# Optimization experiments

Measured on AMD Instinct MI355X. Metric: run time of the kernel, lower is better.

## Reference

```python
import jax, jax.numpy as jnp
import numpy as np

EPS = 1e-5
K_NN = 16

def _lin1d(x, W, b):
    # 1x1 Conv1d: x (B,C,N) -> (B,O,N)
    return jnp.einsum('oc,bcn->bon', W, x) + b[None, :, None]

def _lin2d(x, W, b):
    # 1x1 Conv2d: x (B,C,N,K) -> (B,O,N,K)
    return jnp.einsum('oc,bcnk->bonk', W, x) + b[None, :, None, None]

def _bn2d(x, gamma, beta):
    # train-mode BatchNorm2d over (B, N, K) per channel
    mean = jnp.mean(x, axis=(0, 2, 3), keepdims=True)
    var = jnp.var(x, axis=(0, 2, 3), keepdims=True)
    xh = (x - mean) * jax.lax.rsqrt(var + EPS)
    return gamma[None, :, None, None] * xh + beta[None, :, None, None]

def _knn_idx(pq, ps, k):
    # pq (B,3,N), ps (B,3,M) -> idx (B,N,K) of k nearest support points
    d2 = (jnp.sum(pq * pq, axis=1)[:, :, None]
          + jnp.sum(ps * ps, axis=1)[:, None, :]
          - 2.0 * jnp.einsum('bcn,bcm->bnm', pq, ps))
    _, idx = jax.lax.top_k(-d2, k)
    return idx

def _group(x, idx):
    # x (B,C,M), idx (B,N,K) -> (B,C,N,K)
    return jnp.take_along_axis(x[:, :, None, :], idx[:, None, :, :], axis=3)

def setup_inputs() -> dict:
    key = jax.random.key(0)
    ks = jax.random.split(key, 20)
    B, C, D, N, M, H = 4, 128, 64, 2048, 2048, 256
    s = lambda k, shape, scale: (jax.random.normal(k, shape, dtype=jnp.float32) * scale)
    return {
        'pq': s(ks[0], (B, 3, N), 1.0),
        'fq': s(ks[1], (B, C, N), 1.0),
        'ps': s(ks[2], (B, 3, M), 1.0),
        'fs': s(ks[3], (B, C, M), 1.0),
        'Wq': s(ks[4], (D, C), 0.05), 'bq': jnp.zeros((D,), jnp.float32),
        'Wk': s(ks[5], (D, C), 0.05), 'bk': jnp.zeros((D,), jnp.float32),
        'Wv': s(ks[6], (D, C), 0.05), 'bv': jnp.zeros((D,), jnp.float32),
        'Wp1': s(ks[7], (D, 3), 0.2), 'bp1': jnp.zeros((D,), jnp.float32),
        'gp': jnp.ones((D,), jnp.float32), 'btp': jnp.zeros((D,), jnp.float32),
        'Wp2': s(ks[8], (D, D), 0.05), 'bp2': jnp.zeros((D,), jnp.float32),
        'Wa1': s(ks[9], (H, D), 0.05), 'ba1': jnp.zeros((H,), jnp.float32),
        'ga': jnp.ones((H,), jnp.float32), 'bta': jnp.zeros((H,), jnp.float32),
        'Wa2': s(ks[10], (D, H), 0.05), 'ba2': jnp.zeros((D,), jnp.float32),
        'We': s(ks[11], (C, D), 0.05), 'be': jnp.zeros((C,), jnp.float32),
    }

def reference(pq, fq, ps, fs, Wq, bq, Wk, bk, Wv, bv,
              Wp1, bp1, gp, btp, Wp2, bp2,
              Wa1, ba1, ga, bta, Wa2, ba2, We, be):
    identity = fq
    q = _lin1d(fq, Wq, bq)          # (B,D,N)
    k = _lin1d(fs, Wk, bk)          # (B,D,M)
    v = _lin1d(fs, Wv, bv)          # (B,D,M)
    idx = _knn_idx(pq, ps, K_NN)    # (B,N,K)
    key_g = _group(k, idx)          # (B,D,N,K)
    qk_rel = q[:, :, :, None] - key_g
    pos_rel = pq[:, :, :, None] - _group(ps, idx)  # (B,3,N,K)
    # pos_mlp: conv-bn-relu-conv
    pe = _lin2d(pos_rel, Wp1, bp1)
    pe = jax.nn.relu(_bn2d(pe, gp, btp))
    pe = _lin2d(pe, Wp2, bp2)       # (B,D,N,K)
    # attn_mlp: conv-bn-relu-conv
    a = _lin2d(qk_rel + pe, Wa1, ba1)
    a = jax.nn.relu(_bn2d(a, ga, bta))
    a = _lin2d(a, Wa2, ba2)         # (B,D,N,K)
    attn = jax.nn.softmax(a, axis=-1)
    val = _group(v, idx) + pe       # (B,D,N,K)
    agg = jnp.einsum('bcnk,bcnk->bcn', attn, val)
    return _lin1d(agg, We, be) + identity
```

## Files before the change

kernel.cpp:

```cpp
#include <hip/hip_runtime.h>
#include <stdint.h>

#define NN 2048
#define MM 2048
#define NSAMP 131072

typedef float  fv4 __attribute__((ext_vector_type(4)));
typedef short  bfv8 __attribute__((ext_vector_type(8)));
typedef short  bfv4 __attribute__((ext_vector_type(4)));
typedef unsigned short u16;
typedef unsigned long long u64;

__device__ inline u16 f2bf(float x){
  unsigned u = __float_as_uint(x);
  return (u16)((u + 0x7FFFu + ((u>>16)&1u)) >> 16);
}
__device__ inline float bf2f(u16 u){ return __uint_as_float(((unsigned)u)<<16); }
__device__ inline bfv8 ld8f(const float* __restrict__ p){
  fv4 a = *(const fv4*)p;
  fv4 b = *(const fv4*)(p + 4);
  bfv8 r;
  r[0]=(short)f2bf(a.x); r[1]=(short)f2bf(a.y); r[2]=(short)f2bf(a.z); r[3]=(short)f2bf(a.w);
  r[4]=(short)f2bf(b.x); r[5]=(short)f2bf(b.y); r[6]=(short)f2bf(b.z); r[7]=(short)f2bf(b.w);
  return r;
}
#define MFMA16 __builtin_amdgcn_mfma_f32_16x16x32_bf16

__global__ __launch_bounds__(256) void k_qkv(
    const float* __restrict__ fq, const float* __restrict__ fs,
    const float* __restrict__ Wq, const float* __restrict__ Wk, const float* __restrict__ Wv,
    const float* __restrict__ bq, const float* __restrict__ bk, const float* __restrict__ bv,
    const float* __restrict__ ps,
    float* __restrict__ qT, float* __restrict__ kT, float* __restrict__ vT,
    fv4* __restrict__ psP) {
  __shared__ u16 tile[2][32 * 136];
  int bid = blockIdx.x;
  int b = bid >> 6, p0 = (bid & 63) * 32;
  int t = threadIdx.x;
  int w = t >> 6, l = t & 63, lq = l >> 4, ln = l & 15;
  {
    int gid = bid * 256 + t;
    if (gid < 8192) { int bb = gid >> 11, m = gid & 2047;
      float x = ps[(bb*3+0)*MM + m], y = ps[(bb*3+1)*MM + m], z = ps[(bb*3+2)*MM + m];
      fv4 p; p.x = x; p.y = y; p.z = z; p.w = x*x + y*y + z*z;
      psP[gid] = p; }
  }
  {
    int cq = t >> 3, n4 = (t & 7) * 4;
    #pragma unroll
    for (int it = 0; it < 4; ++it) {
      int c = it * 32 + cq;
      fv4 vq = *(const fv4*)&fq[(b*128 + c)*2048 + p0 + n4];
      fv4 vs = *(const fv4*)&fs[(b*128 + c)*2048 + p0 + n4];
      #pragma unroll
      for (int j = 0; j < 4; ++j) {
        tile[0][(n4 + j)*136 + c] = f2bf(vq[j]);
        tile[1][(n4 + j)*136 + c] = f2bf(vs[j]);
      }
    }
  }
  bfv8 A[3][4];
  #pragma unroll
  for (int mat = 0; mat < 3; ++mat) {
    const float* W = mat == 0 ? Wq : (mat == 1 ? Wk : Wv);
    #pragma unroll
    for (int kk = 0; kk < 4; ++kk)
      A[mat][kk] = ld8f(W + (w*16 + ln)*128 + kk*32 + lq*8);
  }
  __syncthreads();
  fv4 acc[3][2];
  #pragma unroll
  for (int mat = 0; mat < 3; ++mat) {
    const u16* tl = tile[mat == 0 ? 0 : 1];
    #pragma unroll
    for (int nt = 0; nt < 2; ++nt) {
      fv4 a = {0.f,0.f,0.f,0.f};
      #pragma unroll
      for (int kk = 0; kk < 4; ++kk) {
        bfv8 bb = *(const bfv8*)&tl[(nt*16 + ln)*136 + kk*32 + lq*8];
        a = MFMA16(A[mat][kk], bb, a, 0, 0, 0);
      }
      acc[mat][nt] = a;
    }
  }
  #pragma unroll
  for (int mat = 0; mat < 3; ++mat) {
    float* dst = mat == 0 ? qT : (mat == 1 ? kT : vT);
    const float* bia = mat == 0 ? bq : (mat == 1 ? bk : bv);
    fv4 bq4 = *(const fv4*)&bia[w*16 + lq*4];
    #pragma unroll
    for (int nt = 0; nt < 2; ++nt) {
      fv4 o = acc[mat][nt] + bq4;
      *(fv4*)&dst[(b*NN + p0 + nt*16 + ln)*64 + w*16 + lq*4] = o;
    }
  }
}

__global__ __launch_bounds__(256) void k_knn(
    const float* __restrict__ pq, const fv4* __restrict__ psP,
    int* __restrict__ idxb, float* __restrict__ posPart) {
  __shared__ u64 list[4][512];
  __shared__ u64 win[4][16];
  __shared__ int cnt[4];
  __shared__ float sacc[4][9];

  const int t = threadIdx.x, w = t >> 6, lane = t & 63;
  const int qi = blockIdx.x * 4 + w;
  const int b = qi >> 11, n = qi & 2047;
  const float* pqb = pq + b * 3 * NN;
  const fv4* psb = psP + b * 2048;
  const float qx = pqb[n], qy = pqb[NN + n], qz = pqb[2 * NN + n];
  const float qq = qx * qx + qy * qy + qz * qz;

  unsigned key[32];
  unsigned bkey = 0xFFFFFFFFu; unsigned bj = 0;
  #pragma unroll
  for (int j = 0; j < 32; ++j) {
    fv4 P = psb[lane + 64*j];
    float d2 = qq + P.w - 2.f * (qx * P.x + qy * P.y + qz * P.z);
    unsigned bu = __float_as_uint(d2);
    bu = (bu & 0x80000000u) ? ~bu : (bu | 0x80000000u);
    key[j] = bu;
    if (bu < bkey) { bkey = bu; bj = (unsigned)j; }
  }
  u64 e = (((u64)bkey) << 32) | (unsigned)(lane + 64*(int)bj);

  #pragma unroll
  for (int k = 2; k <= 64; k <<= 1) {
    #pragma unroll
    for (int j = k >> 1; j > 0; j >>= 1) {
      u64 x = __shfl_xor(e, j, 64);
      u64 lo = e < x ? e : x, hi = e < x ? x : e;
      bool up = ((lane & k) == 0);
      bool takeLo = (((lane & j) == 0) == up);
      e = takeLo ? lo : hi;
    }
  }
  const u64 thr = __shfl(e, 15, 64);
  const unsigned T32 = (unsigned)(thr >> 32);

  if (lane == 0) cnt[w] = 0;
  #pragma unroll
  for (int j = 0; j < 32; ++j) {
    if (key[j] <= T32) {
      int p = atomicAdd(&cnt[w], 1);
      if (p < 512) list[w][p] = (((u64)key[j]) << 32) | (unsigned)(lane + 64*j);
    }
  }
  const int C = *(volatile int*)&cnt[w];

  u64 myWin = 0;
  if (C <= 64) {
    u64 v = (lane < C) ? list[w][lane] : ~0ULL;
    #pragma unroll
    for (int k = 2; k <= 64; k <<= 1) {
      #pragma unroll
      for (int j = k >> 1; j > 0; j >>= 1) {
        u64 x = __shfl_xor(v, j, 64);
        u64 lo = v < x ? v : x, hi = v < x ? x : v;
        bool up = ((lane & k) == 0);
        bool takeLo = (((lane & j) == 0) == up);
        v = takeLo ? lo : hi;
      }
    }
    myWin = v;
  } else if (C <= 128) {
    u64 e0 = list[w][lane];
    u64 e1 = (64 + lane < C) ? list[w][64 + lane] : ~0ULL;
    #pragma unroll
    for (unsigned k = 2; k <= 128; k <<= 1) {
      #pragma unroll
      for (unsigned j = k >> 1; j > 0; j >>= 1) {
        if (j < 64) {
          u64 x0 = __shfl_xor(e0, (int)j, 64);
          u64 x1 = __shfl_xor(e1, (int)j, 64);
          bool lower = ((lane & j) == 0);
          bool up0 = (k == 128) ? true : ((lane & k) == 0);
          bool up1 = (k == 128) ? true : ((k == 64) ? false : ((lane & k) == 0));
          e0 = (lower == up0) ? (e0 < x0 ? e0 : x0) : (e0 < x0 ? x0 : e0);
          e1 = (lower == up1) ? (e1 < x1 ? e1 : x1) : (e1 < x1 ? x1 : e1);
        } else {
          u64 lo = e0 < e1 ? e0 : e1, hi = e0 < e1 ? e1 : e0;
          e0 = lo; e1 = hi;
        }
      }
    }
    myWin = e0;
  } else {
    int Cc = C > 512 ? 512 : C;
    for (int i = lane; i < 512; i += 64)
      if (i >= Cc) list[w][i] = ~0ULL;
    for (int r = 0; r < 16; ++r) {
      u64 mv = ~0ULL;
      #pragma unroll
      for (int s5 = 0; s5 < 8; ++s5) {
        u64 x = list[w][s5*64 + lane];
        mv = x < mv ? x : mv;
      }
      #pragma unroll
      for (int off = 1; off <= 32; off <<= 1) {
        u64 x = __shfl_xor(mv, off, 64);
        mv = x < mv ? x : mv;
      }
      #pragma unroll
      for (int s5 = 0; s5 < 8; ++s5)
        if (list[w][s5*64 + lane] == mv) list[w][s5*64 + lane] = ~0ULL;
      if (lane == 0) win[w][r] = mv;
    }
    if (lane < 16) myWin = win[w][lane];
  }

  if (lane < 16) {
    unsigned m = (unsigned)(myWin & 0xFFFFFFFFu);
    idxb[qi * 16 + lane] = (int)m;
    fv4 P = psb[m];
    float r0 = qx - P.x, r1 = qy - P.y, r2 = qz - P.z;
    float s[9];
    s[0] = r0; s[1] = r1; s[2] = r2;
    s[3] = r0*r0; s[4] = r0*r1; s[5] = r0*r2;
    s[6] = r1*r1; s[7] = r1*r2; s[8] = r2*r2;
    #pragma unroll
    for (int off = 1; off <= 8; off <<= 1)
      #pragma unroll
      for (int i = 0; i < 9; ++i) s[i] += __shfl_xor(s[i], off, 64);
    if (lane == 0)
      #pragma unroll
      for (int i = 0; i < 9; ++i) sacc[w][i] = s[i];
  }
  __syncthreads();
  if (t < 9) posPart[blockIdx.x * 12 + t]
      = sacc[0][t] + sacc[1][t] + sacc[2][t] + sacc[3][t];
}

__global__ __launch_bounds__(256) void k_posfinal(
    const float* __restrict__ Wp1, const float* __restrict__ bp1,
    const float* __restrict__ gp, const float* __restrict__ btp,
    const float* __restrict__ posPart, float* __restrict__ Wp1f, float* __restrict__ bp1f) {
  __shared__ float red[4][9];
  __shared__ float st[9];
  int t = threadIdx.x;
  int w = t >> 6, lane = t & 63;
  float s[9];
  #pragma unroll
  for (int i = 0; i < 9; ++i) s[i] = 0.f;
  #pragma unroll
  for (int it = 0; it < 8; ++it) {
    const float* p = posPart + (it * 256 + t) * 12;
    fv4 a = *(const fv4*)p;
    fv4 b4 = *(const fv4*)(p + 4);
    float c8 = p[8];
    s[0]+=a.x; s[1]+=a.y; s[2]+=a.z; s[3]+=a.w;
    s[4]+=b4.x; s[5]+=b4.y; s[6]+=b4.z; s[7]+=b4.w;
    s[8]+=c8;
  }
  #pragma unroll
  for (int off = 32; off > 0; off >>= 1)
    #pragma unroll
    for (int i = 0; i < 9; ++i) s[i] += __shfl_xor(s[i], off, 64);
  if (lane == 0)
    #pragma unroll
    for (int i = 0; i < 9; ++i) red[w][i] = s[i];
  __syncthreads();
  if (t < 9) st[t] = red[0][t] + red[1][t] + red[2][t] + red[3][t];
  __syncthreads();
  if (t < 64) {
    int d = t;
    const float invN = 1.f / (float)NSAMP;
    float m0 = st[0]*invN, m1 = st[1]*invN, m2 = st[2]*invN;
    float C00 = st[3]*invN - m0*m0, C01 = st[4]*invN - m0*m1, C02 = st[5]*invN - m0*m2;
    float C11 = st[6]*invN - m1*m1, C12 = st[7]*invN - m1*m2, C22 = st[8]*invN - m2*m2;
    float w0 = Wp1[d*3], w1 = Wp1[d*3+1], w2 = Wp1[d*3+2];
    float mean = w0*m0 + w1*m1 + w2*m2 + bp1[d];
    float var = w0*w0*C00 + w1*w1*C11 + w2*w2*C22 + 2.f*(w0*w1*C01 + w0*w2*C02 + w1*w2*C12);
    float scale = gp[d] * rsqrtf(var + 1e-5f);
    Wp1f[d*3]   = scale * w0;
    Wp1f[d*3+1] = scale * w1;
    Wp1f[d*3+2] = scale * w2;
    bp1f[d] = btp[d] + scale * (bp1[d] - mean);
  }
}

__global__ __launch_bounds__(256) void k_ystats(
    const float* __restrict__ pq, const float* __restrict__ ps,
    const float* __restrict__ qT, const float* __restrict__ kT,
    const int* __restrict__ idxb,
    const float* __restrict__ Wp1f, const float* __restrict__ bp1f,
    const float* __restrict__ Wp2, const float* __restrict__ bp2,
    float* __restrict__ Gpart, float* __restrict__ ySumPart) {
  __shared__ __align__(16) unsigned char smem[21760];
  u16*   hp   = (u16*)smem;
  u16*   y2   = (u16*)(smem + 9216);
  float* r3   = (float*)(smem + 18432);
  float* qc   = (float*)(smem + 19200);
  int*   idxA = (int*)(smem + 20224);
  float* sWp1 = (float*)(smem + 20480);
  float* sbp1 = (float*)(smem + 21248);
  float* sbp2 = (float*)(smem + 21504);

  const int t = threadIdx.x;
  const int w = t >> 6, l = t & 63, lq = l >> 4, ln = l & 15;
  const int d0 = 16*w + lq*4;

  if (t < 192) sWp1[t] = Wp1f[t];
  if (t < 64){ sbp1[t] = bp1f[t]; sbp2[t] = bp2[t]; }

  bfv8 Ape[2];
  #pragma unroll
  for (int kk = 0; kk < 2; ++kk)
    Ape[kk] = ld8f(Wp2 + (16*w + ln)*64 + kk*32 + lq*8);

  fv4 gacc[4];
  #pragma unroll
  for (int nt = 0; nt < 4; ++nt) gacc[nt] = (fv4){0.f,0.f,0.f,0.f};
  float ys[4] = {0.f, 0.f, 0.f, 0.f};
  __syncthreads();

  for (int ch = 0; ch < 4; ++ch) {
    const int p0 = blockIdx.x * 16 + ch * 4;
    const int b  = p0 >> 11;
    const int bN = b * 2048;
    if (t < 64) idxA[t] = idxb[p0*16 + t];
    qc[t] = qT[(p0 + (t>>6))*64 + (t & 63)];
    __syncthreads();
    if (t < 192) { int c = t >> 6, s = t & 63; int n = (p0 + (s>>4)) & 2047;
      r3[c*64 + s] = pq[(b*3+c)*NN + n] - ps[(b*3+c)*MM + idxA[s]]; }
    __syncthreads();
    { int s = t >> 2, iq = t & 3;
      float r0 = r3[s], r1 = r3[64+s], r2 = r3[128+s];
      u16 tmp[16];
      #pragma unroll
      for (int e = 0; e < 16; ++e) { int i = iq*16 + e;
        float v = sbp1[i] + sWp1[i*3]*r0 + sWp1[i*3+1]*r1 + sWp1[i*3+2]*r2;
        tmp[e] = f2bf(fmaxf(v, 0.f)); }
      *(bfv8*)&hp[s*72 + iq*16]     = *(const bfv8*)&tmp[0];
      *(bfv8*)&hp[s*72 + iq*16 + 8] = *(const bfv8*)&tmp[8];
    }
    __syncthreads();
    {
      fv4 pe[4];
      #pragma unroll
      for (int nt = 0; nt < 4; ++nt) {
        fv4 acc = {0.f,0.f,0.f,0.f};
        #pragma unroll
        for (int kk = 0; kk < 2; ++kk) {
          bfv8 bb = *(const bfv8*)&hp[(nt*16 + ln)*72 + kk*32 + lq*8];
          acc = MFMA16(Ape[kk], bb, acc, 0, 0, 0);
        }
        pe[nt] = acc;
      }
      fv4 bp2q = *(const fv4*)&sbp2[d0];
      #pragma unroll
      for (int nt = 0; nt < 4; ++nt) {
        int s = nt*16 + ln;
        int mi = idxA[s];
        fv4 kg = *(const fv4*)(kT + (bN + mi)*64 + d0);
        fv4 qv = *(const fv4*)&qc[nt*64 + d0];
        fv4 yv = qv - kg + pe[nt] + bp2q;
        #pragma unroll
        for (int r = 0; r < 4; ++r) { y2[(d0 + r)*72 + s] = f2bf(yv[r]); ys[r] += yv[r]; }
      }
    }
    __syncthreads();
    #pragma unroll
    for (int kk = 0; kk < 2; ++kk) {
      bfv8 aa = *(const bfv8*)&y2[(16*w + ln)*72 + kk*32 + lq*8];
      #pragma unroll
      for (int nt = 0; nt < 4; ++nt) {
        bfv8 bb = *(const bfv8*)&y2[(nt*16 + ln)*72 + kk*32 + lq*8];
        gacc[nt] = MFMA16(aa, bb, gacc[nt], 0, 0, 0);
      }
    }
    __syncthreads();
  }
  #pragma unroll
  for (int nt = 0; nt < 4; ++nt)
    #pragma unroll
    for (int r = 0; r < 4; ++r)
      Gpart[blockIdx.x*4096 + (16*w + lq*4 + r)*64 + nt*16 + ln] = gacc[nt][r];
  #pragma unroll
  for (int off = 1; off <= 8; off <<= 1) {
    #pragma unroll
    for (int r = 0; r < 4; ++r) ys[r] += __shfl_xor(ys[r], off, 64);
  }
  if (ln == 0) {
    #pragma unroll
    for (int r = 0; r < 4; ++r) ySumPart[blockIdx.x*64 + d0 + r] = ys[r];
  }
}

__global__ __launch_bounds__(256) void k_gred(
    const float* __restrict__ Gpart, const float* __restrict__ ySumPart,
    float* __restrict__ G, float* __restrict__ ySum) {
  __shared__ float red[256];
  int bid = blockIdx.x, t = threadIdx.x;
  int tj = t & 63, st = t >> 6;
  if (bid < 64) {
    int j = bid * 64 + tj;
    float s = 0.f;
    for (int p = st * 128; p < st * 128 + 128; ++p)
      s += Gpart[p*4096 + j];
    red[st * 64 + tj] = s;
    __syncthreads();
    if (t < 64)
      G[bid * 64 + t] = red[t] + red[64 + t] + red[128 + t] + red[192 + t];
  } else {
    float s = 0.f;
    for (int p = st * 128; p < st * 128 + 128; ++p)
      s += ySumPart[p*64 + tj];
    red[st * 64 + tj] = s;
    __syncthreads();
    if (t < 64)
      ySum[t] = red[t] + red[64 + t] + red[128 + t] + red[192 + t];
  }
}

__global__ __launch_bounds__(256) void k_attnfinal(
    const float* __restrict__ Wa1, const float* __restrict__ ba1,
    const float* __restrict__ ga, const float* __restrict__ bta,
    const float* __restrict__ ySum, const float* __restrict__ G,
    u16* __restrict__ Wa1fbf, float* __restrict__ ba1f) {
  __shared__ float red[256];
  __shared__ float mu[64];
  __shared__ float sc[1];
  int h = blockIdx.x, t = threadIdx.x;
  const float invN = 1.f / (float)NSAMP;
  if (t < 64) mu[t] = ySum[t] * invN;
  __syncthreads();
  float acc = 0.f;
  #pragma unroll
  for (int e = 0; e < 16; ++e) {
    int pi = t*16 + e, i = pi >> 6, j = pi & 63;
    float cov = G[pi]*invN - mu[i]*mu[j];
    acc += Wa1[h*64 + i] * Wa1[h*64 + j] * cov;
  }
  red[t] = acc;
  __syncthreads();
  for (int s = 128; s > 0; s >>= 1) { if (t < s) red[t] += red[t + s]; __syncthreads(); }
  float var = red[0];
  __syncthreads();
  red[t] = (t < 64) ? Wa1[h*64 + t] * mu[t] : 0.f;
  __syncthreads();
  for (int s = 128; s > 0; s >>= 1) { if (t < s) red[t] += red[t + s]; __syncthreads(); }
  if (t == 0) {
    float mean  = red[0] + ba1[h];
    float scale = ga[h] * rsqrtf(var + 1e-5f);
    sc[0] = scale;
    ba1f[h] = bta[h] + scale * (ba1[h] - mean);
  }
  __syncthreads();
  if (t < 64) Wa1fbf[h*64 + t] = f2bf(sc[0] * Wa1[h*64 + t]);
}

__global__ __launch_bounds__(256) void k_main(
    const float* __restrict__ pq, const float* __restrict__ ps,
    const float* __restrict__ qT, const float* __restrict__ kT, const float* __restrict__ vT,
    const int* __restrict__ idxb,
    const float* __restrict__ Wp1f, const float* __restrict__ bp1f,
    const float* __restrict__ Wp2, const float* __restrict__ bp2,
    const u16* __restrict__ Wa1fbf, const float* __restrict__ ba1f,
    const float* __restrict__ Wa2, const float* __restrict__ ba2,
    const float* __restrict__ We, const float* __restrict__ be,
    const float* __restrict__ fq,
    u16* __restrict__ aggbf, float* __restrict__ out) {
  __shared__ __align__(16) unsigned char smem[65024];
  u16*   hp   = (u16*)smem;
  u16*   ha   = (u16*)smem;
  u16*   ylds = (u16*)(smem + 33792);
  float* at   = (float*)(smem + 33792);
  u16*   vt   = (u16*)(smem + 51200);
  float* r3   = (float*)(smem + 60416);
  float* qc   = (float*)(smem + 61184);
  int*   idxA = (int*)(smem + 62208);
  float* sWp1 = (float*)(smem + 62464);
  float* sbp1 = (float*)(smem + 63232);
  float* sbp2 = (float*)(smem + 63488);
  float* sba1 = (float*)(smem + 63744);
  float* sba2 = (float*)(smem + 64768);

  const int t = threadIdx.x;
  const int w = t >> 6, l = t & 63, lq = l >> 4, ln = l & 15;
  const int d0 = 16*w + lq*4;

  if (t < 192) sWp1[t] = Wp1f[t];
  if (t < 64){ sbp1[t] = bp1f[t]; sbp2[t] = bp2[t]; sba2[t] = ba2[t]; }
  sba1[t] = ba1f[t];

  bfv8 Ape[2], A1[4][2], A2[8];
  #pragma unroll
  for (int kk = 0; kk < 2; ++kk)
    Ape[kk] = ld8f(Wp2 + (16*w + ln)*64 + kk*32 + lq*8);
  #pragma unroll
  for (int mt = 0; mt < 4; ++mt)
    #pragma unroll
    for (int kk = 0; kk < 2; ++kk)
      A1[mt][kk] = *(const bfv8*)(Wa1fbf + (64*w + mt*16 + ln)*64 + kk*32 + lq*8);
  #pragma unroll
  for (int kk = 0; kk < 8; ++kk)
    A2[kk] = ld8f(Wa2 + (16*w + ln)*256 + kk*32 + lq*8);
  __syncthreads();

  for (int ch = 0; ch < 4; ++ch) {
    const int p0 = blockIdx.x * 16 + ch * 4;
    const int b  = p0 >> 11;
    const int bN = b * 2048;
    if (t < 64) idxA[t] = idxb[p0*16 + t];
    qc[t] = qT[(p0 + (t>>6))*64 + (t & 63)];
    __syncthreads();
    if (t < 192) { int c = t >> 6, s = t & 63; int n = (p0 + (s>>4)) & 2047;
      r3[c*64 + s] = pq[(b*3+c)*NN + n] - ps[(b*3+c)*MM + idxA[s]]; }
    __syncthreads();
    { int s = t >> 2, iq = t & 3;
      float r0 = r3[s], r1 = r3[64+s], r2 = r3[128+s];
      u16 tmp[16];
      #pragma unroll
      for (int e = 0; e < 16; ++e) { int i = iq*16 + e;
        float v = sbp1[i] + sWp1[i*3]*r0 + sWp1[i*3+1]*r1 + sWp1[i*3+2]*r2;
        tmp[e] = f2bf(fmaxf(v, 0.f)); }
      *(bfv8*)&hp[s*72 + iq*16]     = *(const bfv8*)&tmp[0];
      *(bfv8*)&hp[s*72 + iq*16 + 8] = *(const bfv8*)&tmp[8];
    }
    __syncthreads();
    {
      fv4 pe[4];
      #pragma unroll
      for (int nt = 0; nt < 4; ++nt) {
        fv4 acc = {0.f,0.f,0.f,0.f};
        #pragma unroll
        for (int kk = 0; kk < 2; ++kk) {
          bfv8 bb = *(const bfv8*)&hp[(nt*16 + ln)*72 + kk*32 + lq*8];
          acc = MFMA16(Ape[kk], bb, acc, 0, 0, 0);
        }
        pe[nt] = acc;
      }
      fv4 bp2q = *(const fv4*)&sbp2[d0];
      #pragma unroll
      for (int nt = 0; nt < 4; ++nt) {
        int s = nt*16 + ln;
        int mi = idxA[s];
        fv4 kg = *(const fv4*)(kT + (bN + mi)*64 + d0);
        fv4 vg = *(const fv4*)(vT + (bN + mi)*64 + d0);
        fv4 qv = *(const fv4*)&qc[nt*64 + d0];
        fv4 pv = pe[nt] + bp2q;
        fv4 yv = qv - kg + pv;
        fv4 vv = vg + pv;
        u16 yp[4], vp[4];
        #pragma unroll
        for (int r = 0; r < 4; ++r) { yp[r] = f2bf(yv[r]); vp[r] = f2bf(vv[r]); }
        *(bfv4*)&ylds[s*72 + d0] = *(const bfv4*)yp;
        *(bfv4*)&vt[s*72 + d0]   = *(const bfv4*)vp;
      }
    }
    __syncthreads();
    #pragma unroll
    for (int nt = 0; nt < 4; ++nt) {
      int s = nt*16 + ln;
      bfv8 b0 = *(const bfv8*)&ylds[s*72 + lq*8];
      bfv8 b1 = *(const bfv8*)&ylds[s*72 + 32 + lq*8];
      #pragma unroll
      for (int mt = 0; mt < 4; ++mt) {
        fv4 acc = {0.f,0.f,0.f,0.f};
        acc = MFMA16(A1[mt][0], b0, acc, 0, 0, 0);
        acc = MFMA16(A1[mt][1], b1, acc, 0, 0, 0);
        int h0 = 64*w + mt*16 + lq*4;
        fv4 bq = *(const fv4*)&sba1[h0];
        u16 hv[4];
        #pragma unroll
        for (int r = 0; r < 4; ++r) hv[r] = f2bf(fmaxf(acc[r] + bq[r], 0.f));
        *(bfv4*)&ha[s*264 + h0] = *(const bfv4*)hv;
      }
    }
    __syncthreads();
    {
      fv4 acc2[4];
      #pragma unroll
      for (int nt = 0; nt < 4; ++nt) acc2[nt] = (fv4){0.f,0.f,0.f,0.f};
      #pragma unroll
      for (int kk = 0; kk < 8; ++kk) {
        #pragma unroll
        for (int nt = 0; nt < 4; ++nt) {
          bfv8 bb = *(const bfv8*)&ha[(nt*16 + ln)*264 + kk*32 + lq*8];
          acc2[nt] = MFMA16(A2[kk], bb, acc2[nt], 0, 0, 0);
        }
      }
      fv4 ba2q = *(const fv4*)&sba2[d0];
      #pragma unroll
      for (int nt = 0; nt < 4; ++nt) {
        int s = nt*16 + ln;
        fv4 o = acc2[nt] + ba2q;
        *(fv4*)&at[s*68 + d0] = o;
      }
    }
    __syncthreads();
    {
      int dd = t & 63, pt = t >> 6;
      float a[16];
      #pragma unroll
      for (int k = 0; k < 16; ++k) a[k] = at[(pt*16 + k)*68 + dd];
      float mx = a[0];
      #pragma unroll
      for (int k = 1; k < 16; ++k) mx = fmaxf(mx, a[k]);
      float sum = 0.f, num = 0.f;
      #pragma unroll
      for (int k = 0; k < 16; ++k) {
        float e = __expf(a[k] - mx);
        sum += e;
        num += e * bf2f(vt[(pt*16 + k)*72 + dd]);
      }
      aggbf[(p0 + pt)*64 + dd] = f2bf(num / sum);
    }
    __syncthreads();
  }
  {
    const int P0 = blockIdx.x * 16;
    const int b  = P0 >> 11;
    const int n0 = P0 & 2047;
    bfv8 EA[2][2];
    #pragma unroll
    for (int mt = 0; mt < 2; ++mt)
      #pragma unroll
      for (int kk = 0; kk < 2; ++kk)
        EA[mt][kk] = ld8f(We + ((w*2 + mt)*16 + ln)*64 + kk*32 + lq*8);
    const u16* bp = aggbf + (P0 + ln)*64;
    bfv8 b0 = *(const bfv8*)(bp + lq*8);
    bfv8 b1 = *(const bfv8*)(bp + 32 + lq*8);
    fv4 eacc[2];
    #pragma unroll
    for (int mt = 0; mt < 2; ++mt) {
      fv4 a = {0.f,0.f,0.f,0.f};
      a = MFMA16(EA[mt][0], b0, a, 0, 0, 0);
      a = MFMA16(EA[mt][1], b1, a, 0, 0, 0);
      eacc[mt] = a;
    }
    #pragma unroll
    for (int mt = 0; mt < 2; ++mt) {
      int c0 = (w*2 + mt)*16 + lq*4;
      fv4 bev = *(const fv4*)&be[c0];
      #pragma unroll
      for (int r = 0; r < 4; ++r) {
        int c = c0 + r;
        int o = (b*128 + c)*2048 + n0 + ln;
        out[o] = eacc[mt][r] + bev[r] + fq[o];
      }
    }
  }
}

extern "C" void kernel_launch(void* const* d_in, const int* in_sizes, int n_in,
                              void* d_out, int out_size, void* d_ws, size_t ws_size,
                              hipStream_t stream) {
  (void)in_sizes; (void)n_in; (void)out_size; (void)ws_size;
  const float* pq  = (const float*)d_in[0];
  const float* fq  = (const float*)d_in[1];
  const float* ps  = (const float*)d_in[2];
  const float* fs  = (const float*)d_in[3];
  const float* Wq  = (const float*)d_in[4];  const float* bq  = (const float*)d_in[5];
  const float* Wk  = (const float*)d_in[6];  const float* bk  = (const float*)d_in[7];
  const float* Wv  = (const float*)d_in[8];  const float* bv  = (const float*)d_in[9];
  const float* Wp1 = (const float*)d_in[10]; const float* bp1 = (const float*)d_in[11];
  const float* gp  = (const float*)d_in[12]; const float* btp = (const float*)d_in[13];
  const float* Wp2 = (const float*)d_in[14]; const float* bp2 = (const float*)d_in[15];
  const float* Wa1 = (const float*)d_in[16]; const float* ba1 = (const float*)d_in[17];
  const float* ga  = (const float*)d_in[18]; const float* bta = (const float*)d_in[19];
  const float* Wa2 = (const float*)d_in[20]; const float* ba2 = (const float*)d_in[21];
  const float* We  = (const float*)d_in[22]; const float* be  = (const float*)d_in[23];
  float* ws = (float*)d_ws;
  float* qT    = ws;
  float* kT    = ws + 524288;
  float* vT    = ws + 1048576;
  u16*   aggbf = (u16*)(ws + 1572864);
  int*   idxb  = (int*)(ws + 1835008);
  fv4*   psP   = (fv4*)(ws + 1966080);
  float* Wp1f  = ws + 1998848;
  float* bp1f  = ws + 1999040;
  float* ba1f  = ws + 1999104;
  float* G     = ws + 1999360;
  float* ySum  = ws + 2003456;
  float* ySumP = ws + 2003520;
  u16*   Wa1fbf = (u16*)(ws + 2036288);
  float* posPart = ws + 2044480;
  float* Gpart   = ws + 2069056;
  float* out   = (float*)d_out;

  k_qkv<<<256, 256, 0, stream>>>(fq, fs, Wq, Wk, Wv, bq, bk, bv, ps,
                                 qT, kT, vT, psP);
  k_knn<<<2048, 256, 0, stream>>>(pq, psP, idxb, posPart);
  k_posfinal<<<1, 256, 0, stream>>>(Wp1, bp1, gp, btp, posPart, Wp1f, bp1f);
  k_ystats<<<512, 256, 0, stream>>>(pq, ps, qT, kT, idxb, Wp1f, bp1f, Wp2, bp2,
                                    Gpart, ySumP);
  k_gred<<<65, 256, 0, stream>>>(Gpart, ySumP, G, ySum);
  k_attnfinal<<<256, 256, 0, stream>>>(Wa1, ba1, ga, bta, ySum, G, Wa1fbf, ba1f);
  k_main<<<512, 256, 0, stream>>>(pq, ps, qT, kT, vT, idxb, Wp1f, bp1f, Wp2, bp2,
                                  Wa1fbf, ba1f, Wa2, ba2, We, be, fq, aggbf, out);
}
```

Before: 212.8 us.

## Fold tiny finalize kernels into producers via last-block and grid sync

Removes the single-block k_posfinal launch by having the last finishing k_knn block, detected with an atomic counter reset in k_qkv, reduce posPart and compute the folded BN weights. Merges k_gred and k_attnfinal into one cooperative kernel with a grid-wide sync between the reduction and the per-head finalize. The aim is to cut launch gaps and tail latency of tiny kernels. In exchange it adds atomics, fences and a grid barrier, and relies on cooperative launch co-residency of 256 blocks.

After: 467.9 us. 120% more time.

```diff
diff --git a/kernel.cpp b/kernel.cpp
--- a/kernel.cpp
+++ b/kernel.cpp
@@ -1,5 +1,8 @@
 #include <hip/hip_runtime.h>
+#include <hip/hip_cooperative_groups.h>
 #include <stdint.h>
+
+namespace cg = cooperative_groups;
 
 #define NN 2048
 #define MM 2048
@@ -32,12 +35,13 @@
     const float* __restrict__ bq, const float* __restrict__ bk, const float* __restrict__ bv,
     const float* __restrict__ ps,
     float* __restrict__ qT, float* __restrict__ kT, float* __restrict__ vT,
-    fv4* __restrict__ psP) {
+    fv4* __restrict__ psP, int* __restrict__ knnCtr) {
   __shared__ u16 tile[2][32 * 136];
   int bid = blockIdx.x;
   int b = bid >> 6, p0 = (bid & 63) * 32;
   int t = threadIdx.x;
   int w = t >> 6, l = t & 63, lq = l >> 4, ln = l & 15;
+  if (bid == 0 && t == 0) *knnCtr = 0;
   {
     int gid = bid * 256 + t;
     if (gid < 8192) { int bb = gid >> 11, m = gid & 2047;
@@ -98,11 +102,17 @@
 
 __global__ __launch_bounds__(256) void k_knn(
     const float* __restrict__ pq, const fv4* __restrict__ psP,
-    int* __restrict__ idxb, float* __restrict__ posPart) {
+    int* __restrict__ idxb, float* __restrict__ posPart,
+    const float* __restrict__ Wp1, const float* __restrict__ bp1,
+    const float* __restrict__ gp, const float* __restrict__ btp,
+    float* __restrict__ Wp1f, float* __restrict__ bp1f,
+    int* __restrict__ knnCtr) {
   __shared__ u64 list[4][512];
   __shared__ u64 win[4][16];
   __shared__ int cnt[4];
   __shared__ float sacc[4][9];
+  __shared__ float stf[9];
+  __shared__ int lastBlk;
 
   const int t = threadIdx.x, w = t >> 6, lane = t & 63;
   const int qi = blockIdx.x * 4 + w;
@@ -230,53 +240,51 @@
   __syncthreads();
   if (t < 9) posPart[blockIdx.x * 12 + t]
       = sacc[0][t] + sacc[1][t] + sacc[2][t] + sacc[3][t];
-}
-
-__global__ __launch_bounds__(256) void k_posfinal(
-    const float* __restrict__ Wp1, const float* __restrict__ bp1,
-    const float* __restrict__ gp, const float* __restrict__ btp,
-    const float* __restrict__ posPart, float* __restrict__ Wp1f, float* __restrict__ bp1f) {
-  __shared__ float red[4][9];
-  __shared__ float st[9];
-  int t = threadIdx.x;
-  int w = t >> 6, lane = t & 63;
-  float s[9];
-  #pragma unroll
-  for (int i = 0; i < 9; ++i) s[i] = 0.f;
-  #pragma unroll
-  for (int it = 0; it < 8; ++it) {
-    const float* p = posPart + (it * 256 + t) * 12;
-    fv4 a = *(const fv4*)p;
-    fv4 b4 = *(const fv4*)(p + 4);
-    float c8 = p[8];
-    s[0]+=a.x; s[1]+=a.y; s[2]+=a.z; s[3]+=a.w;
-    s[4]+=b4.x; s[5]+=b4.y; s[6]+=b4.z; s[7]+=b4.w;
-    s[8]+=c8;
-  }
-  #pragma unroll
-  for (int off = 32; off > 0; off >>= 1)
-    #pragma unroll
-    for (int i = 0; i < 9; ++i) s[i] += __shfl_xor(s[i], off, 64);
-  if (lane == 0)
-    #pragma unroll
-    for (int i = 0; i < 9; ++i) red[w][i] = s[i];
-  __syncthreads();
-  if (t < 9) st[t] = red[0][t] + red[1][t] + red[2][t] + red[3][t];
-  __syncthreads();
-  if (t < 64) {
-    int d = t;
-    const float invN = 1.f / (float)NSAMP;
-    float m0 = st[0]*invN, m1 = st[1]*invN, m2 = st[2]*invN;
-    float C00 = st[3]*invN - m0*m0, C01 = st[4]*invN - m0*m1, C02 = st[5]*invN - m0*m2;
-    float C11 = st[6]*invN - m1*m1, C12 = st[7]*invN - m1*m2, C22 = st[8]*invN - m2*m2;
-    float w0 = Wp1[d*3], w1 = Wp1[d*3+1], w2 = Wp1[d*3+2];
-    float mean = w0*m0 + w1*m1 + w2*m2 + bp1[d];
-    float var = w0*w0*C00 + w1*w1*C11 + w2*w2*C22 + 2.f*(w0*w1*C01 + w0*w2*C02 + w1*w2*C12);
-    float scale = gp[d] * rsqrtf(var + 1e-5f);
-    Wp1f[d*3]   = scale * w0;
-    Wp1f[d*3+1] = scale * w1;
-    Wp1f[d*3+2] = scale * w2;
-    bp1f[d] = btp[d] + scale * (bp1[d] - mean);
+
+  __threadfence();
+  __syncthreads();
+  if (t == 0) {
+    int old = __hip_atomic_fetch_add(knnCtr, 1, __ATOMIC_ACQ_REL,
+                                     __HIP_MEMORY_SCOPE_AGENT);
+    lastBlk = (old == 2047) ? 1 : 0;
+  }
+  __syncthreads();
+  if (lastBlk) {
+    float s[9];
+    #pragma unroll
+    for (int i = 0; i < 9; ++i) s[i] = 0.f;
+    #pragma unroll
+    for (int it = 0; it < 8; ++it) {
+      const float* p = posPart + (it * 256 + t) * 12;
+      #pragma unroll
+      for (int i = 0; i < 9; ++i)
+        s[i] += __hip_atomic_load(p + i, __ATOMIC_RELAXED, __HIP_MEMORY_SCOPE_AGENT);
+    }
+    #pragma unroll
+    for (int off = 32; off > 0; off >>= 1)
+      #pragma unroll
+      for (int i = 0; i < 9; ++i) s[i] += __shfl_xor(s[i], off, 64);
+    if ((t & 63) == 0)
+      #pragma unroll
+      for (int i = 0; i < 9; ++i) sacc[t >> 6][i] = s[i];
+    __syncthreads();
+    if (t < 9) stf[t] = sacc[0][t] + sacc[1][t] + sacc[2][t] + sacc[3][t];
+    __syncthreads();
+    if (t < 64) {
+      int d = t;
+      const float invN = 1.f / (float)NSAMP;
+      float m0 = stf[0]*invN, m1 = stf[1]*invN, m2 = stf[2]*invN;
+      float C00 = stf[3]*invN - m0*m0, C01 = stf[4]*invN - m0*m1, C02 = stf[5]*invN - m0*m2;
+      float C11 = stf[6]*invN - m1*m1, C12 = stf[7]*invN - m1*m2, C22 = stf[8]*invN - m2*m2;
+      float w0 = Wp1[d*3], w1 = Wp1[d*3+1], w2 = Wp1[d*3+2];
+      float mean = w0*m0 + w1*m1 + w2*m2 + bp1[d];
+      float var = w0*w0*C00 + w1*w1*C11 + w2*w2*C22 + 2.f*(w0*w1*C01 + w0*w2*C02 + w1*w2*C12);
+      float scale = gp[d] * rsqrtf(var + 1e-5f);
+      Wp1f[d*3]   = scale * w0;
+      Wp1f[d*3+1] = scale * w1;
+      Wp1f[d*3+2] = scale * w2;
+      bp1f[d] = btp[d] + scale * (bp1[d] - mean);
+    }
   }
 }
 
@@ -388,13 +396,18 @@
   }
 }
 
-__global__ __launch_bounds__(256) void k_gred(
+__global__ __launch_bounds__(256) void k_gredattn(
     const float* __restrict__ Gpart, const float* __restrict__ ySumPart,
-    float* __restrict__ G, float* __restrict__ ySum) {
+    float* __restrict__ G, float* __restrict__ ySum,
+    const float* __restrict__ Wa1, const float* __restrict__ ba1,
+    const float* __restrict__ ga, const float* __restrict__ bta,
+    u16* __restrict__ Wa1fbf, float* __restrict__ ba1f) {
   __shared__ float red[256];
+  __shared__ float mu[64];
+  __shared__ float sc[1];
   int bid = blockIdx.x, t = threadIdx.x;
-  int tj = t & 63, st = t >> 6;
   if (bid < 64) {
+    int tj = t & 63, st = t >> 6;
     int j = bid * 64 + tj;
     float s = 0.f;
     for (int p = st * 128; p < st * 128 + 128; ++p)
@@ -403,7 +416,8 @@
     __syncthreads();
     if (t < 64)
       G[bid * 64 + t] = red[t] + red[64 + t] + red[128 + t] + red[192 + t];
-  } else {
+  } else if (bid == 64) {
+    int tj = t & 63, st = t >> 6;
     float s = 0.f;
     for (int p = st * 128; p < st * 128 + 128; ++p)
       s += ySumPart[p*64 + tj];
@@ -412,17 +426,8 @@
     if (t < 64)
       ySum[t] = red[t] + red[64 + t] + red[128 + t] + red[192 + t];
   }
-}
-
-__global__ __launch_bounds__(256) void k_attnfinal(
-    const float* __restrict__ Wa1, const float* __restrict__ ba1,
-    const float* __restrict__ ga, const float* __restrict__ bta,
-    const float* __restrict__ ySum, const float* __restrict__ G,
-    u16* __restrict__ Wa1fbf, float* __restrict__ ba1f) {
-  __shared__ float red[256];
-  __shared__ float mu[64];
-  __shared__ float sc[1];
-  int h = blockIdx.x, t = threadIdx.x;
+  cg::this_grid().sync();
+  int h = bid;
   const float invN = 1.f / (float)NSAMP;
   if (t < 64) mu[t] = ySum[t] * invN;
   __syncthreads();
@@ -679,16 +684,22 @@
   u16*   Wa1fbf = (u16*)(ws + 2036288);
   float* posPart = ws + 2044480;
   float* Gpart   = ws + 2069056;
+  int*   knnCtr  = (int*)(ws + 4166208);
   float* out   = (float*)d_out;
 
   k_qkv<<<256, 256, 0, stream>>>(fq, fs, Wq, Wk, Wv, bq, bk, bv, ps,
-                                 qT, kT, vT, psP);
-  k_knn<<<2048, 256, 0, stream>>>(pq, psP, idxb, posPart);
-  k_posfinal<<<1, 256, 0, stream>>>(Wp1, bp1, gp, btp, posPart, Wp1f, bp1f);
+                                 qT, kT, vT, psP, knnCtr);
+  k_knn<<<2048, 256, 0, stream>>>(pq, psP, idxb, posPart,
+                                  Wp1, bp1, gp, btp, Wp1f, bp1f, knnCtr);
   k_ystats<<<512, 256, 0, stream>>>(pq, ps, qT, kT, idxb, Wp1f, bp1f, Wp2, bp2,
                                     Gpart, ySumP);
-  k_gred<<<65, 256, 0, stream>>>(Gpart, ySumP, G, ySum);
-  k_attnfinal<<<256, 256, 0, stream>>>(Wa1, ba1, ga, bta, ySum, G, Wa1fbf, ba1f);
+  {
+    void* args[] = { (void*)&Gpart, (void*)&ySumP, (void*)&G, (void*)&ySum,
+                     (void*)&Wa1, (void*)&ba1, (void*)&ga, (void*)&bta,
+                     (void*)&Wa1fbf, (void*)&ba1f };
+    hipLaunchCooperativeKernel((const void*)k_gredattn, dim3(256), dim3(256),
+                               args, 0, stream);
+  }
   k_main<<<512, 256, 0, stream>>>(pq, ps, qT, kT, vT, idxb, Wp1f, bp1f, Wp2, bp2,
                                   Wa1fbf, ba1f, Wa2, ba2, We, be, fq, aggbf, out);
 }
```

## Merge QKV projection and kNN kernels into one launch with block-range dispatch

Applied to the files above, without the earlier changes.

Combines the QKV projection kernel and the kNN kernel into a single launch, with the first 256 blocks doing the projection and the rest doing kNN, sharing one union shared-memory buffer. The precomputed packed support-point array (xyz plus squared norm) is removed, so kNN reads the three coordinate planes directly and recomputes the norm per candidate. This removes one launch and the dependency between the two stages, letting them overlap. In exchange the kNN inner loop issues three scalar loads instead of one vector load and does a little extra arithmetic.

Result: faster. 205.0 us, median of 2 (-3.7%).

```diff
diff --git a/kernel.cpp b/kernel.cpp
--- a/kernel.cpp
+++ b/kernel.cpp
@@ -26,89 +26,84 @@
 }
 #define MFMA16 __builtin_amdgcn_mfma_f32_16x16x32_bf16
 
-__global__ __launch_bounds__(256) void k_qkv(
+__global__ __launch_bounds__(256) void k_front(
     const float* __restrict__ fq, const float* __restrict__ fs,
     const float* __restrict__ Wq, const float* __restrict__ Wk, const float* __restrict__ Wv,
     const float* __restrict__ bq, const float* __restrict__ bk, const float* __restrict__ bv,
-    const float* __restrict__ ps,
+    const float* __restrict__ pq, const float* __restrict__ ps,
     float* __restrict__ qT, float* __restrict__ kT, float* __restrict__ vT,
-    fv4* __restrict__ psP) {
-  __shared__ u16 tile[2][32 * 136];
-  int bid = blockIdx.x;
-  int b = bid >> 6, p0 = (bid & 63) * 32;
-  int t = threadIdx.x;
-  int w = t >> 6, l = t & 63, lq = l >> 4, ln = l & 15;
-  {
-    int gid = bid * 256 + t;
-    if (gid < 8192) { int bb = gid >> 11, m = gid & 2047;
-      float x = ps[(bb*3+0)*MM + m], y = ps[(bb*3+1)*MM + m], z = ps[(bb*3+2)*MM + m];
-      fv4 p; p.x = x; p.y = y; p.z = z; p.w = x*x + y*y + z*z;
-      psP[gid] = p; }
-  }
-  {
-    int cq = t >> 3, n4 = (t & 7) * 4;
-    #pragma unroll
-    for (int it = 0; it < 4; ++it) {
-      int c = it * 32 + cq;
-      fv4 vq = *(const fv4*)&fq[(b*128 + c)*2048 + p0 + n4];
-      fv4 vs = *(const fv4*)&fs[(b*128 + c)*2048 + p0 + n4];
-      #pragma unroll
-      for (int j = 0; j < 4; ++j) {
-        tile[0][(n4 + j)*136 + c] = f2bf(vq[j]);
-        tile[1][(n4 + j)*136 + c] = f2bf(vs[j]);
-      }
-    }
-  }
-  bfv8 A[3][4];
-  #pragma unroll
-  for (int mat = 0; mat < 3; ++mat) {
-    const float* W = mat == 0 ? Wq : (mat == 1 ? Wk : Wv);
-    #pragma unroll
-    for (int kk = 0; kk < 4; ++kk)
-      A[mat][kk] = ld8f(W + (w*16 + ln)*128 + kk*32 + lq*8);
-  }
-  __syncthreads();
-  fv4 acc[3][2];
-  #pragma unroll
-  for (int mat = 0; mat < 3; ++mat) {
-    const u16* tl = tile[mat == 0 ? 0 : 1];
-    #pragma unroll
-    for (int nt = 0; nt < 2; ++nt) {
-      fv4 a = {0.f,0.f,0.f,0.f};
-      #pragma unroll
-      for (int kk = 0; kk < 4; ++kk) {
-        bfv8 bb = *(const bfv8*)&tl[(nt*16 + ln)*136 + kk*32 + lq*8];
-        a = MFMA16(A[mat][kk], bb, a, 0, 0, 0);
-      }
-      acc[mat][nt] = a;
-    }
-  }
-  #pragma unroll
-  for (int mat = 0; mat < 3; ++mat) {
-    float* dst = mat == 0 ? qT : (mat == 1 ? kT : vT);
-    const float* bia = mat == 0 ? bq : (mat == 1 ? bk : bv);
-    fv4 bq4 = *(const fv4*)&bia[w*16 + lq*4];
-    #pragma unroll
-    for (int nt = 0; nt < 2; ++nt) {
-      fv4 o = acc[mat][nt] + bq4;
-      *(fv4*)&dst[(b*NN + p0 + nt*16 + ln)*64 + w*16 + lq*4] = o;
-    }
-  }
-}
-
-__global__ __launch_bounds__(256) void k_knn(
-    const float* __restrict__ pq, const fv4* __restrict__ psP,
     int* __restrict__ idxb, float* __restrict__ posPart) {
-  __shared__ u64 list[4][512];
-  __shared__ u64 win[4][16];
-  __shared__ int cnt[4];
-  __shared__ float sacc[4][9];
-
-  const int t = threadIdx.x, w = t >> 6, lane = t & 63;
-  const int qi = blockIdx.x * 4 + w;
+  __shared__ __align__(16) unsigned char smem[17408];
+  const int t = threadIdx.x;
+
+  if (blockIdx.x < 256) {
+    u16* tile = (u16*)smem;
+    int bid = blockIdx.x;
+    int b = bid >> 6, p0 = (bid & 63) * 32;
+    int w = t >> 6, l = t & 63, lq = l >> 4, ln = l & 15;
+    {
+      int cq = t >> 3, n4 = (t & 7) * 4;
+      #pragma unroll
+      for (int it = 0; it < 4; ++it) {
+        int c = it * 32 + cq;
+        fv4 vq = *(const fv4*)&fq[(b*128 + c)*2048 + p0 + n4];
+        fv4 vs = *(const fv4*)&fs[(b*128 + c)*2048 + p0 + n4];
+        #pragma unroll
+        for (int j = 0; j < 4; ++j) {
+          tile[0*32*136 + (n4 + j)*136 + c] = f2bf(vq[j]);
+          tile[1*32*136 + (n4 + j)*136 + c] = f2bf(vs[j]);
+        }
+      }
+    }
+    bfv8 A[3][4];
+    #pragma unroll
+    for (int mat = 0; mat < 3; ++mat) {
+      const float* W = mat == 0 ? Wq : (mat == 1 ? Wk : Wv);
+      #pragma unroll
+      for (int kk = 0; kk < 4; ++kk)
+        A[mat][kk] = ld8f(W + (w*16 + ln)*128 + kk*32 + lq*8);
+    }
+    __syncthreads();
+    fv4 acc[3][2];
+    #pragma unroll
+    for (int mat = 0; mat < 3; ++mat) {
+      const u16* tl = tile + (mat == 0 ? 0 : 32*136);
+      #pragma unroll
+      for (int nt = 0; nt < 2; ++nt) {
+        fv4 a = {0.f,0.f,0.f,0.f};
+        #pragma unroll
+        for (int kk = 0; kk < 4; ++kk) {
+          bfv8 bb = *(const bfv8*)&tl[(nt*16 + ln)*136 + kk*32 + lq*8];
+          a = MFMA16(A[mat][kk], bb, a, 0, 0, 0);
+        }
+        acc[mat][nt] = a;
+      }
+    }
+    #pragma unroll
+    for (int mat = 0; mat < 3; ++mat) {
+      float* dst = mat == 0 ? qT : (mat == 1 ? kT : vT);
+      const float* bia = mat == 0 ? bq : (mat == 1 ? bk : bv);
+      fv4 bq4 = *(const fv4*)&bia[w*16 + lq*4];
+      #pragma unroll
+      for (int nt = 0; nt < 2; ++nt) {
+        fv4 o = acc[mat][nt] + bq4;
+        *(fv4*)&dst[(b*NN + p0 + nt*16 + ln)*64 + w*16 + lq*4] = o;
+      }
+    }
+    return;
+  }
+
+  u64*   list = (u64*)smem;
+  u64*   win  = (u64*)(smem + 16384);
+  int*   cnt  = (int*)(smem + 16896);
+  float* sacc = (float*)(smem + 16912);
+
+  const int kbid = blockIdx.x - 256;
+  const int w = t >> 6, lane = t & 63;
+  const int qi = kbid * 4 + w;
   const int b = qi >> 11, n = qi & 2047;
   const float* pqb = pq + b * 3 * NN;
-  const fv4* psb = psP + b * 2048;
+  const float* psb = ps + b * 3 * MM;
   const float qx = pqb[n], qy = pqb[NN + n], qz = pqb[2 * NN + n];
   const float qq = qx * qx + qy * qy + qz * qz;
 
@@ -116,8 +111,10 @@
   unsigned bkey = 0xFFFFFFFFu; unsigned bj = 0;
   #pragma unroll
   for (int j = 0; j < 32; ++j) {
-    fv4 P = psb[lane + 64*j];
-    float d2 = qq + P.w - 2.f * (qx * P.x + qy * P.y + qz * P.z);
+    int m = lane + 64*j;
+    float x = psb[m], y = psb[MM + m], z = psb[2*MM + m];
+    float w2 = x*x + y*y + z*z;
+    float d2 = qq + w2 - 2.f * (qx * x + qy * y + qz * z);
     unsigned bu = __float_as_uint(d2);
     bu = (bu & 0x80000000u) ? ~bu : (bu | 0x80000000u);
     key[j] = bu;
@@ -144,14 +141,14 @@
   for (int j = 0; j < 32; ++j) {
     if (key[j] <= T32) {
       int p = atomicAdd(&cnt[w], 1);
-      if (p < 512) list[w][p] = (((u64)key[j]) << 32) | (unsigned)(lane + 64*j);
+      if (p < 512) list[w*512 + p] = (((u64)key[j]) << 32) | (unsigned)(lane + 64*j);
     }
   }
   const int C = *(volatile int*)&cnt[w];
 
   u64 myWin = 0;
   if (C <= 64) {
-    u64 v = (lane < C) ? list[w][lane] : ~0ULL;
+    u64 v = (lane < C) ? list[w*512 + lane] : ~0ULL;
     #pragma unroll
     for (int k = 2; k <= 64; k <<= 1) {
       #pragma unroll
@@ -165,8 +162,8 @@
     }
     myWin = v;
   } else if (C <= 128) {
-    u64 e0 = list[w][lane];
-    u64 e1 = (64 + lane < C) ? list[w][64 + lane] : ~0ULL;
+    u64 e0 = list[w*512 + lane];
+    u64 e1 = (64 + lane < C) ? list[w*512 + 64 + lane] : ~0ULL;
     #pragma unroll
     for (unsigned k = 2; k <= 128; k <<= 1) {
       #pragma unroll
@@ -189,12 +186,12 @@
   } else {
     int Cc = C > 512 ? 512 : C;
     for (int i = lane; i < 512; i += 64)
-      if (i >= Cc) list[w][i] = ~0ULL;
+      if (i >= Cc) list[w*512 + i] = ~0ULL;
     for (int r = 0; r < 16; ++r) {
       u64 mv = ~0ULL;
       #pragma unroll
       for (int s5 = 0; s5 < 8; ++s5) {
-        u64 x = list[w][s5*64 + lane];
+        u64 x = list[w*512 + s5*64 + lane];
         mv = x < mv ? x : mv;
       }
       #pragma unroll
@@ -204,17 +201,17 @@
       }
       #pragma unroll
       for (int s5 = 0; s5 < 8; ++s5)
-        if (list[w][s5*64 + lane] == mv) list[w][s5*64 + lane] = ~0ULL;
-      if (lane == 0) win[w][r] = mv;
-    }
-    if (lane < 16) myWin = win[w][lane];
+        if (list[w*512 + s5*64 + lane] == mv) list[w*512 + s5*64 + lane] = ~0ULL;
+      if (lane == 0) win[w*16 + r] = mv;
+    }
+    if (lane < 16) myWin = win[w*16 + lane];
   }
 
   if (lane < 16) {
     unsigned m = (unsigned)(myWin & 0xFFFFFFFFu);
     idxb[qi * 16 + lane] = (int)m;
-    fv4 P = psb[m];
-    float r0 = qx - P.x, r1 = qy - P.y, r2 = qz - P.z;
+    float x = psb[m], y = psb[MM + m], z = psb[2*MM + m];
+    float r0 = qx - x, r1 = qy - y, r2 = qz - z;
     float s[9];
     s[0] = r0; s[1] = r1; s[2] = r2;
     s[3] = r0*r0; s[4] = r0*r1; s[5] = r0*r2;
@@ -225,11 +222,11 @@
       for (int i = 0; i < 9; ++i) s[i] += __shfl_xor(s[i], off, 64);
     if (lane == 0)
       #pragma unroll
-      for (int i = 0; i < 9; ++i) sacc[w][i] = s[i];
-  }
-  __syncthreads();
-  if (t < 9) posPart[blockIdx.x * 12 + t]
-      = sacc[0][t] + sacc[1][t] + sacc[2][t] + sacc[3][t];
+      for (int i = 0; i < 9; ++i) sacc[w*9 + i] = s[i];
+  }
+  __syncthreads();
+  if (t < 9) posPart[kbid * 12 + t]
+      = sacc[0*9 + t] + sacc[1*9 + t] + sacc[2*9 + t] + sacc[3*9 + t];
 }
 
 __global__ __launch_bounds__(256) void k_posfinal(
@@ -669,7 +666,6 @@
   float* vT    = ws + 1048576;
   u16*   aggbf = (u16*)(ws + 1572864);
   int*   idxb  = (int*)(ws + 1835008);
-  fv4*   psP   = (fv4*)(ws + 1966080);
   float* Wp1f  = ws + 1998848;
   float* bp1f  = ws + 1999040;
   float* ba1f  = ws + 1999104;
@@ -681,9 +677,8 @@
   float* Gpart   = ws + 2069056;
   float* out   = (float*)d_out;
 
-  k_qkv<<<256, 256, 0, stream>>>(fq, fs, Wq, Wk, Wv, bq, bk, bv, ps,
-                                 qT, kT, vT, psP);
-  k_knn<<<2048, 256, 0, stream>>>(pq, psP, idxb, posPart);
+  k_front<<<2304, 256, 0, stream>>>(fq, fs, Wq, Wk, Wv, bq, bk, bv, pq, ps,
+                                    qT, kT, vT, idxb, posPart);
   k_posfinal<<<1, 256, 0, stream>>>(Wp1, bp1, gp, btp, posPart, Wp1f, bp1f);
   k_ystats<<<512, 256, 0, stream>>>(pq, ps, qT, kT, idxb, Wp1f, bp1f, Wp2, bp2,
                                     Gpart, ySumP);
```
